# Optimization experiments

Hardware: AMD Instinct MI355X
Metric: run time of the kernel (lower is better)

## Reference

```python
import jax, jax.numpy as jnp
import numpy as np
import math

L, B, S, D, H, R = 4, 2, 1024, 1024, 16, 4
DH = D // H
SCALE = 1.0 / math.sqrt(DH)
EPS = 1e-5  # torch LayerNorm default


def _xavier(key, shape):
    fan_in, fan_out = shape[-2], shape[-1]
    bound = math.sqrt(6.0 / (fan_in + fan_out))
    return jax.random.uniform(key, shape, minval=-bound, maxval=bound, dtype=jnp.float32)


def setup_inputs() -> dict:
    key = jax.random.key(0)
    ks = jax.random.split(key, 12)
    f32 = jnp.float32
    return {
        "x": jax.random.normal(ks[0], (B, S, D), f32),
        "sigma": jnp.full((L,), 0.1, f32),
        "U": jax.random.normal(ks[1], (L, D, R), f32),
        "V": jax.random.normal(ks[2], (L, R, D), f32),
        "Wqkv1": _xavier(ks[3], (L, D, 3 * D)),
        "Wqkv2": _xavier(ks[4], (L, D, 3 * D)),
        "Wp1": _xavier(ks[5], (L, D // 2, D)),
        "bp1": jnp.zeros((L, D), f32),
        "Wp2": _xavier(ks[6], (L, D // 2, D)),
        "bp2": jnp.zeros((L, D), f32),
        "Wo": _xavier(ks[7], (L, D, D)),
        "bo": jnp.zeros((L, D), f32),
        "g_out": jnp.ones((L, D), f32), "b_out": jnp.zeros((L, D), f32),
        "g1": jnp.ones((L, D), f32), "b1": jnp.zeros((L, D), f32),
        "g2": jnp.ones((L, D), f32), "b2": jnp.zeros((L, D), f32),
        "Wm1": _xavier(ks[8], (L, D, 4 * D)),
        "bm1": jnp.zeros((L, 4 * D), f32),
        "Wm2": _xavier(ks[9], (L, 4 * D, D)),
        "bm2": jnp.zeros((L, D), f32),
        "gf": jnp.ones((D,), f32), "bf": jnp.zeros((D,), f32),
    }


def _ln(h, g, b):
    m = h.mean(-1, keepdims=True)
    v = ((h - m) ** 2).mean(-1, keepdims=True)
    return (h - m) * jax.lax.rsqrt(v + EPS) * g + b


def _heads(t):  # [B,S,D] -> [B,H,S,DH]
    return t.reshape(B, S, H, DH).transpose(0, 2, 1, 3)


def _forward(x, sigma, U, V, Wqkv1, Wqkv2, Wp1, bp1, Wp2, bp2, Wo, bo,
             g_out, b_out, g1, b1, g2, b2, Wm1, bm1, Wm2, bm2, gf, bf):
    params = (sigma, U, V, Wqkv1, Wqkv2, Wp1, bp1, Wp2, bp2, Wo, bo,
              g_out, b_out, g1, b1, g2, b2, Wm1, bm1, Wm2, bm2)

    def layer(xc, p):
        (sig, U_, V_, Wq1, Wq2, Wp1_, bp1_, Wp2_, bp2_, Wo_, bo_,
         gO, bO, g1_, b1_, g2_, b2_, Wm1_, bm1_, Wm2_, bm2_) = p
        h = _ln(xc, g1_, b1_)
        # svd_adapt = (sigma * (U @ V)).sum(-1) broadcast over batch/seq
        adapt = (sig * (U_ @ V_)).sum(-1)  # [D]
        a = h + adapt
        x1, x2 = jnp.split(a, 2, axis=-1)
        x1 = x1 @ Wp1_ + bp1_
        x2 = x2 @ Wp2_ + bp2_
        q1, k1, v1 = jnp.split(x1 @ Wq1, 3, axis=-1)
        q2, k2, v2 = jnp.split(x2 @ Wq2, 3, axis=-1)
        q1, k1, v1, q2, k2, v2 = map(_heads, (q1, k1, v1, q2, k2, v2))
        a1 = jax.nn.softmax(jnp.einsum('bhqd,bhkd->bhqk', q1, k1) * SCALE, axis=-1)
        a2 = jax.nn.softmax(jnp.einsum('bhqd,bhkd->bhqk', q2, k2) * SCALE, axis=-1)
        diff = a1 - a2
        # (diff@v1 + diff@v2)/2 == diff @ ((v1+v2)/2)
        out = jnp.einsum('bhqk,bhkd->bhqd', diff, (v1 + v2) * 0.5)
        out = out.transpose(0, 2, 1, 3).reshape(B, S, D)
        out = _ln(out @ Wo_ + bo_, gO, bO)
        xc = xc + out
        h2 = _ln(xc, g2_, b2_)
        xc = xc + (jax.nn.gelu(h2 @ Wm1_ + bm1_, approximate=False) @ Wm2_ + bm2_)
        return xc, None

    x, _ = jax.lax.scan(layer, x, params)
    return _ln(x, gf, bf)


def reference(x, sigma, U, V, Wqkv1, Wqkv2, Wp1, bp1, Wp2, bp2, Wo, bo,
              g_out, b_out, g1, b1, g2, b2, Wm1, bm1, Wm2, bm2, gf, bf):
    return _forward(x, sigma, U, V, Wqkv1, Wqkv2, Wp1, bp1, Wp2, bp2, Wo, bo,
                    g_out, b_out, g1, b1, g2, b2, Wm1, bm1, Wm2, bm2, gf, bf)
```

## Files before the change

### kernel.cpp

```cpp
#include <hip/hip_runtime.h>
#include <math.h>

typedef unsigned short u16;
typedef short bf16x8 __attribute__((ext_vector_type(8)));
typedef float f32x4 __attribute__((ext_vector_type(4)));

__device__ __forceinline__ float bf2f(u16 u){ return __uint_as_float(((unsigned)u)<<16); }
__device__ __forceinline__ u16 f2bf(float f){
  unsigned u = __float_as_uint(f);
  u += 0x7fffu + ((u>>16)&1u);
  return (u16)(u>>16);
}
__device__ __forceinline__ float gelu_f(float x){ return 0.5f*x*(1.0f+erff(x*0.7071067811865476f)); }

__device__ __forceinline__ void gload16(const void* g, void* l){
  __builtin_amdgcn_global_load_lds((const __attribute__((address_space(1))) void*)g,
                                   (__attribute__((address_space(3))) void*)l, 16, 0, 0);
}

__device__ __forceinline__ float block_sum(float v, float* sh){
  #pragma unroll
  for (int o=32;o;o>>=1) v += __shfl_down(v,o,64);
  int w = threadIdx.x>>6, lane = threadIdx.x&63;
  __syncthreads();
  if (lane==0) sh[w]=v;
  __syncthreads();
  return sh[0]+sh[1]+sh[2]+sh[3];
}

template<int FM,int FN,int OF32,int ACC,int ACT>
__global__ __launch_bounds__(256) void gemm2_k(
    const u16* __restrict__ A, const u16* __restrict__ Bm, void* __restrict__ Cv,
    const float* __restrict__ bias,
    int K,int lda,int ldb,int ldc,float alpha,int z0,
    long sAz,long oAb,long oAh, long sBz,long oBb,long oBh, long sCz,long oCb,long oCh)
{
  constexpr int BM = FM*32, BN = FN*32;
  int zz = blockIdx.z; int z = z0+zz; int bb = z>>4, hh = z&15;
  const u16* Ap = A  + (long)zz*sAz + (long)bb*oAb + (long)hh*oAh;
  const u16* Bp = Bm + (long)zz*sBz + (long)bb*oBb + (long)hh*oBh;
  long coff = (long)zz*sCz + (long)bb*oCb + (long)hh*oCh;
  int m0 = blockIdx.y*BM, n0 = blockIdx.x*BN;
  __shared__ __align__(16) u16 As[BM][64];
  __shared__ __align__(16) u16 Bs[BN][64];
  u16* AsF = &As[0][0]; u16* BsF = &Bs[0][0];
  int tid = threadIdx.x, w = tid>>6, l = tid&63;
  int q = l>>4, m16 = l&15;
  int wr = w>>1, wc = w&1;
  int sr  = w*8 + (l>>3);
  int sch = (l&7) ^ ((l>>3)&7);
  int s7  = m16 & 7;

  f32x4 acc[FM][FN];
  #pragma unroll
  for (int i=0;i<FM;i++)
    #pragma unroll
    for (int j=0;j<FN;j++) acc[i][j] = (f32x4){0.f,0.f,0.f,0.f};

  int aRow = wr*(FM*16) + m16;
  int bRow = wc*(FN*16) + m16;

  for (int k0=0;k0<K;k0+=64){
    __syncthreads();
    #pragma unroll
    for (int c=0;c<FM;c++)
      gload16(Ap + (long)(m0 + c*32 + sr)*lda + k0 + sch*8, AsF + c*2048 + w*512);
    #pragma unroll
    for (int c=0;c<FN;c++)
      gload16(Bp + (long)(n0 + c*32 + sr)*ldb + k0 + sch*8, BsF + c*2048 + w*512);
    __syncthreads();
    #pragma unroll
    for (int kh=0;kh<2;kh++){
      bf16x8 afr[FM], bfr[FN];
      #pragma unroll
      for (int i=0;i<FM;i++)
        afr[i] = *(const bf16x8*)(AsF + (aRow + i*16)*64 + (((kh<<2)|q) ^ s7)*8);
      #pragma unroll
      for (int j=0;j<FN;j++)
        bfr[j] = *(const bf16x8*)(BsF + (bRow + j*16)*64 + (((kh<<2)|q) ^ s7)*8);
      #pragma unroll
      for (int i=0;i<FM;i++)
        #pragma unroll
        for (int j=0;j<FN;j++)
          acc[i][j] = __builtin_amdgcn_mfma_f32_16x16x32_bf16(afr[i], bfr[j], acc[i][j], 0,0,0);
    }
  }
  #pragma unroll
  for (int j=0;j<FN;j++){
    int n = n0 + wc*(FN*16) + j*16 + m16;
    float bv = bias ? bias[n] : 0.0f;
    #pragma unroll
    for (int i=0;i<FM;i++){
      #pragma unroll
      for (int r=0;r<4;r++){
        int m = m0 + wr*(FM*16) + i*16 + q*4 + r;
        float v = acc[i][j][r]*alpha + bv;
        if (ACT==1) v = gelu_f(v);
        long ci = coff + (long)m*ldc + n;
        if (OF32){
          float* C = (float*)Cv;
          if (ACC) C[ci] += v; else C[ci] = v;
        } else {
          ((u16*)Cv)[ci] = f2bf(v);
        }
      }
    }
  }
}

__device__ __forceinline__ void flash_stream(
    const u16* Kl, const u16* Vl, u16* Plw,
    bf16x8 qa, bf16x8 qb, int qd, int m16,
    float& mrun, float& lsum, f32x4* O)
{
  int r7 = m16 & 7;
  f32x4 s[4];
  #pragma unroll
  for (int f=0;f<4;f++){
    s[f] = (f32x4){0.f,0.f,0.f,0.f};
    int row = f*16 + m16;
    bf16x8 ka = *(const bf16x8*)(Kl + row*64 + ((qd    ) ^ r7)*8);
    bf16x8 kb = *(const bf16x8*)(Kl + row*64 + ((4 + qd) ^ r7)*8);
    s[f] = __builtin_amdgcn_mfma_f32_16x16x32_bf16(ka, qa, s[f], 0,0,0);
    s[f] = __builtin_amdgcn_mfma_f32_16x16x32_bf16(kb, qb, s[f], 0,0,0);
  }
  float sc[16]; float pmax = -1e30f;
  #pragma unroll
  for (int f=0;f<4;f++)
    #pragma unroll
    for (int r=0;r<4;r++){ float v = s[f][r]*0.125f; sc[f*4+r]=v; pmax = fmaxf(pmax,v); }
  pmax = fmaxf(pmax, __shfl_xor(pmax,16,64));
  pmax = fmaxf(pmax, __shfl_xor(pmax,32,64));
  float mnew = fmaxf(mrun, pmax);
  float corr = expf(mrun - mnew);
  float psum = 0.f;
  #pragma unroll
  for (int f=0;f<4;f++){
    u16 pb[4];
    #pragma unroll
    for (int r=0;r<4;r++){ float e = expf(sc[f*4+r]-mnew); psum += e; pb[r] = f2bf(e); }
    unsigned lo = (unsigned)pb[0] | ((unsigned)pb[1]<<16);
    unsigned hi = (unsigned)pb[2] | ((unsigned)pb[3]<<16);
    uint2 pv; pv.x = lo; pv.y = hi;
    *(uint2*)(Plw + m16*72 + f*16 + qd*4) = pv;
  }
  psum += __shfl_xor(psum,16,64);
  psum += __shfl_xor(psum,32,64);
  lsum = lsum*corr + psum;
  mrun = mnew;
  float cO[4];
  #pragma unroll
  for (int r=0;r<4;r++) cO[r] = __shfl(corr, qd*4 + r, 64);
  #pragma unroll
  for (int f2=0;f2<4;f2++)
    #pragma unroll
    for (int r=0;r<4;r++) O[f2][r] *= cO[r];
  #pragma unroll
  for (int b32=0;b32<2;b32++){
    bf16x8 pa = *(const bf16x8*)(Plw + m16*72 + b32*32 + qd*8);
    #pragma unroll
    for (int f2=0;f2<4;f2++){
      int row = f2*16 + m16;
      bf16x8 vb = *(const bf16x8*)(Vl + row*64 + (((b32<<2)|qd) ^ r7)*8);
      O[f2] = __builtin_amdgcn_mfma_f32_16x16x32_bf16(pa, vb, O[f2], 0,0,0);
    }
  }
}

__global__ __launch_bounds__(256) void flash_k(
    const u16* __restrict__ qkv1, const u16* __restrict__ qkv2,
    const u16* __restrict__ vavgT, u16* __restrict__ outp)
{
  __shared__ __align__(16) u16 K1l[4096];
  __shared__ __align__(16) u16 K2l[4096];
  __shared__ __align__(16) u16 Vl[4096];
  __shared__ __align__(16) u16 Pl[4608];
  int z = blockIdx.y, b = z>>4, h = z&15;
  int q0 = blockIdx.x*64;
  int tid = threadIdx.x, w = tid>>6, l = tid&63;
  int qd = l>>4, m16 = l&15;
  int lr = l>>3;
  int sch = (l&7) ^ lr;
  u16* Plw = Pl + w*1152;

  const u16* q1p = qkv1 + ((long)(b*1024 + q0 + w*16 + m16))*3072 + h*64;
  const u16* q2p = qkv2 + ((long)(b*1024 + q0 + w*16 + m16))*3072 + h*64;
  bf16x8 q1a = *(const bf16x8*)(q1p + qd*8);
  bf16x8 q1b = *(const bf16x8*)(q1p + 32 + qd*8);
  bf16x8 q2a = *(const bf16x8*)(q2p + qd*8);
  bf16x8 q2b = *(const bf16x8*)(q2p + 32 + qd*8);

  const u16* k1base = qkv1 + ((long)(b*1024))*3072 + 1024 + h*64;
  const u16* k2base = qkv2 + ((long)(b*1024))*3072 + 1024 + h*64;
  const u16* vbase  = vavgT + (long)z*65536;

  float m1 = -1e30f, l1 = 0.f, m2 = -1e30f, l2 = 0.f;
  f32x4 O1[4], O2[4];
  #pragma unroll
  for (int f=0;f<4;f++){ O1[f]=(f32x4){0.f,0.f,0.f,0.f}; O2[f]=(f32x4){0.f,0.f,0.f,0.f}; }

  for (int t=0;t<16;t++){
    __syncthreads();
    #pragma unroll
    for (int c2=0;c2<2;c2++){
      int r = c2*32 + w*8 + lr;
      gload16(k1base + (long)(t*64 + r)*3072 + sch*8, K1l + c2*2048 + w*512);
      gload16(k2base + (long)(t*64 + r)*3072 + sch*8, K2l + c2*2048 + w*512);
      gload16(vbase  + (long)r*1024 + t*64 + sch*8,   Vl  + c2*2048 + w*512);
    }
    __syncthreads();
    flash_stream(K1l, Vl, Plw, q1a, q1b, qd, m16, m1, l1, O1);
    flash_stream(K2l, Vl, Plw, q2a, q2b, qd, m16, m2, l2, O2);
  }
  float inv1 = 1.0f/l1, inv2 = 1.0f/l2;
  float i1O[4], i2O[4];
  #pragma unroll
  for (int r=0;r<4;r++){ i1O[r] = __shfl(inv1, qd*4+r, 64); i2O[r] = __shfl(inv2, qd*4+r, 64); }
  #pragma unroll
  for (int f2=0;f2<4;f2++){
    #pragma unroll
    for (int r=0;r<4;r++){
      long idx = ((long)(b*1024 + q0 + w*16 + qd*4 + r))*1024 + h*64 + f2*16 + m16;
      outp[idx] = f2bf(O1[f2][r]*i1O[r] - O2[f2][r]*i2O[r]);
    }
  }
}

__global__ __launch_bounds__(256) void wtc_k(const float* __restrict__ in,
                                             u16* __restrict__ out, int N, int K){
  __shared__ float tile[64][65];
  int bx = blockIdx.x, by = blockIdx.y;
  int t = threadIdx.x, r = t>>6, c = t&63;
  const float* ip = in + (long)(by*64)*N + bx*64;
  #pragma unroll
  for (int i=0;i<16;i++) tile[i*4+r][c] = ip[(long)(i*4+r)*N + c];
  __syncthreads();
  u16* op = out + (long)(bx*64)*K + by*64;
  #pragma unroll
  for (int i=0;i<16;i++) op[(long)(i*4+r)*K + c] = f2bf(tile[c][i*4+r]);
}

template<int ACCXC,int HAS_OUT,int OUTF32>
__global__ __launch_bounds__(256) void ln_k(const float* __restrict__ in,
    const float* __restrict__ g, const float* __restrict__ b,
    float* __restrict__ xc, void* __restrict__ out)
{
  __shared__ float sh[4];
  long row = blockIdx.x;
  int tid = threadIdx.x;
  float x[4];
  #pragma unroll
  for (int i=0;i<4;i++) x[i] = in[row*1024 + tid + 256*i];
  float s = x[0]+x[1]+x[2]+x[3];
  float mean = block_sum(s, sh) * (1.0f/1024.0f);
  float ss = 0.f;
  #pragma unroll
  for (int i=0;i<4;i++){ float d = x[i]-mean; ss += d*d; }
  float var = block_sum(ss, sh) * (1.0f/1024.0f);
  float rstd = rsqrtf(var + 1e-5f);
  #pragma unroll
  for (int i=0;i<4;i++){
    int col = tid + 256*i;
    long idx = row*1024 + col;
    float val = (x[i]-mean)*rstd*g[col];
    if (b) val += b[col];
    if (ACCXC) xc[idx] += val;
    if (HAS_OUT){
      if (OUTF32) ((float*)out)[idx] = val;
      else ((u16*)out)[idx] = f2bf(val);
    }
  }
}

__global__ void cvt_k(const float* __restrict__ x, float* __restrict__ xc){
  long i = (long)blockIdx.x*256 + threadIdx.x;
  xc[i] = x[i];
}

__device__ __forceinline__ unsigned avg2(unsigned a, unsigned b){
  u16 r0 = f2bf(0.5f*(bf2f((u16)(a&0xffff)) + bf2f((u16)(b&0xffff))));
  u16 r1 = f2bf(0.5f*(bf2f((u16)(a>>16))    + bf2f((u16)(b>>16))));
  return (unsigned)r0 | ((unsigned)r1<<16);
}

__global__ __launch_bounds__(256) void vavg_k(const u16* __restrict__ qkv1,
                                              const u16* __restrict__ qkv2,
                                              u16* __restrict__ vavgT){
  __shared__ u16 tile[64][72];
  int z = blockIdx.y, b = z>>4, h = z&15;
  int s0 = blockIdx.x*64;
  int t = threadIdx.x, r = t>>2, seg = t&3;
  const u16* p1 = qkv1 + ((long)(b*1024 + s0 + r))*3072 + 2048 + h*64 + seg*16;
  const u16* p2 = qkv2 + ((long)(b*1024 + s0 + r))*3072 + 2048 + h*64 + seg*16;
  #pragma unroll
  for (int c=0;c<2;c++){
    uint4 a = *(const uint4*)(p1 + c*8);
    uint4 bb = *(const uint4*)(p2 + c*8);
    uint4 o; o.x = avg2(a.x,bb.x); o.y = avg2(a.y,bb.y); o.z = avg2(a.z,bb.z); o.w = avg2(a.w,bb.w);
    *(uint4*)&tile[r][seg*16 + c*8] = o;
  }
  __syncthreads();
  u16 ov[16];
  #pragma unroll
  for (int j=0;j<16;j++) ov[j] = tile[seg*16+j][r];
  uint4 w0, w1;
  w0.x = ov[0]|(ov[1]<<16);  w0.y = ov[2]|(ov[3]<<16);
  w0.z = ov[4]|(ov[5]<<16);  w0.w = ov[6]|(ov[7]<<16);
  w1.x = ov[8]|(ov[9]<<16);  w1.y = ov[10]|(ov[11]<<16);
  w1.z = ov[12]|(ov[13]<<16); w1.w = ov[14]|(ov[15]<<16);
  u16* op = vavgT + (long)z*65536 + (long)r*1024 + s0 + seg*16;
  *(uint4*)op = w0;
  *(uint4*)(op+8) = w1;
}

__global__ void abar_k(const float* __restrict__ sig, const float* __restrict__ U,
                       const float* __restrict__ V, const float* __restrict__ b1,
                       float* __restrict__ abar){
  __shared__ float vs[4];
  int tid = threadIdx.x, w = tid>>6, lane = tid&63;
  float p = 0.f;
  #pragma unroll
  for (int i=0;i<16;i++) p += V[w*1024 + lane + 64*i];
  #pragma unroll
  for (int o=32;o;o>>=1) p += __shfl_down(p,o,64);
  if (lane==0) vs[w] = p;
  __syncthreads();
  float sg = sig[0];
  for (int d=tid; d<1024; d+=256){
    float a = 0.f;
    #pragma unroll
    for (int r=0;r<4;r++) a += U[d*4+r]*vs[r];
    abar[d] = b1[d] + sg*a;
  }
}

__global__ void bar1p_k(const float* __restrict__ abar,
                        const float* __restrict__ Wp1, const float* __restrict__ Wp2,
                        float* __restrict__ bp){
  int n = blockIdx.x*256 + threadIdx.x;
  int kc = blockIdx.y;
  float s1=0.f, s2=0.f;
  for (int j=0;j<32;j++){
    int k = kc*32+j;
    s1 += abar[k]     * Wp1[(long)k*1024 + n];
    s2 += abar[512+k] * Wp2[(long)k*1024 + n];
  }
  bp[kc*2048 + n] = s1; bp[kc*2048 + 1024 + n] = s2;
}
__global__ void bar1r_k(const float* __restrict__ bp,
                        const float* __restrict__ bp1, const float* __restrict__ bp2,
                        float* __restrict__ x1bar, float* __restrict__ x2bar){
  int n = blockIdx.x*256 + threadIdx.x;
  float s1 = bp1[n], s2 = bp2[n];
  for (int kc=0;kc<16;kc++){ s1 += bp[kc*2048+n]; s2 += bp[kc*2048+1024+n]; }
  x1bar[n] = s1; x2bar[n] = s2;
}
__global__ void bar2p_k(const float* __restrict__ xbar, const float* __restrict__ Wq,
                        float* __restrict__ qp){
  int n = blockIdx.x*256 + threadIdx.x;
  int kc = blockIdx.y;
  float s = 0.f;
  for (int j=0;j<32;j++){
    int k = kc*32+j;
    s += xbar[k] * Wq[(long)k*3072 + n];
  }
  qp[kc*1024 + n] = s;
}
__global__ void bar2r_k(const float* __restrict__ qp, float* __restrict__ qbias){
  int m = blockIdx.x*256 + threadIdx.x;
  float s = 0.f;
  if (m < 1024){ for (int kc=0;kc<32;kc++) s += qp[kc*1024 + m]; }
  qbias[m] = s;
}

extern "C" void kernel_launch(void* const* d_in, const int* in_sizes, int n_in,
                              void* d_out, int out_size, void* d_ws, size_t ws_size,
                              hipStream_t stream){
  const float* X    = (const float*)d_in[0];
  const float* SIG  = (const float*)d_in[1];
  const float* U    = (const float*)d_in[2];
  const float* V    = (const float*)d_in[3];
  const float* Wqkv1= (const float*)d_in[4];
  const float* Wqkv2= (const float*)d_in[5];
  const float* Wp1  = (const float*)d_in[6];
  const float* bp1  = (const float*)d_in[7];
  const float* Wp2  = (const float*)d_in[8];
  const float* bp2  = (const float*)d_in[9];
  const float* Wo   = (const float*)d_in[10];
  const float* bo   = (const float*)d_in[11];
  const float* gO   = (const float*)d_in[12];
  const float* bO   = (const float*)d_in[13];
  const float* g1   = (const float*)d_in[14];
  const float* b1   = (const float*)d_in[15];
  const float* g2   = (const float*)d_in[16];
  const float* b2   = (const float*)d_in[17];
  const float* Wm1  = (const float*)d_in[18];
  const float* bm1  = (const float*)d_in[19];
  const float* Wm2  = (const float*)d_in[20];
  const float* bm2  = (const float*)d_in[21];
  const float* gf   = (const float*)d_in[22];
  const float* bfv  = (const float*)d_in[23];
  (void)in_sizes; (void)n_in; (void)out_size; (void)ws_size;

  char* p = (char*)d_ws;
  float* xc     = (float*)(p + 0);
  u16* qkv1     = (u16*)(p + 8388608);
  u16* qkv2     = (u16*)(p + 20971520);
  u16* bufA     = (u16*)(p + 33554432);
  u16* bufB     = (u16*)(p + 37748736);
  u16* bufC     = (u16*)(p + 41943040);
  u16* mid      = (u16*)(p + 46137344);
  float* projout= (float*)(p + 46137344);
  float* abar   = (float*)(p + 71303168);
  float* x1bar  = (float*)(p + 71307264);
  float* x2bar  = (float*)(p + 71311360);
  u16* wpT1     = (u16*)(p + 46137344);
  u16* wpT2     = (u16*)(p + 46137344 + 1048576);
  u16* wqkvT1   = (u16*)(p + 46137344 + 2097152);
  u16* wqkvT2   = (u16*)(p + 46137344 + 8388608);
  float* qbias1 = (float*)(p + 46137344 + 14680064);
  float* qbias2 = (float*)(p + 46137344 + 14692352);
  u16* woT      = (u16*)(p + 8388608);
  u16* wm1T     = (u16*)(p + 8388608 + 2097152);
  u16* wm2T     = (u16*)(p + 8388608 + 10485760);
  float* bp     = (float*)(p + 62914560);
  float* qp     = (float*)(p + 62914560 + 131072);

  u16* a_bf    = bufA; u16* attnout = bufA; u16* h2 = bufA;
  u16* x1w     = bufB;
  u16* x2w     = bufC; u16* vavgT   = bufC;

  cvt_k<<<8192,256,0,stream>>>(X, xc);
  for (int l=0;l<4;l++){
    abar_k<<<1,256,0,stream>>>(SIG+l, U+(long)l*4096, V+(long)l*4096, b1+l*1024, abar);
    bar1p_k<<<dim3(4,16),256,0,stream>>>(abar, Wp1+(long)l*524288, Wp2+(long)l*524288, bp);
    bar1r_k<<<4,256,0,stream>>>(bp, bp1+l*1024, bp2+l*1024, x1bar, x2bar);
    bar2p_k<<<dim3(4,32),256,0,stream>>>(x1bar, Wqkv1+(long)l*3145728, qp);
    bar2r_k<<<12,256,0,stream>>>(qp, qbias1);
    bar2p_k<<<dim3(4,32),256,0,stream>>>(x2bar, Wqkv2+(long)l*3145728, qp);
    bar2r_k<<<12,256,0,stream>>>(qp, qbias2);
    wtc_k<<<dim3(16,8), 256,0,stream>>>(Wp1+(long)l*524288,  wpT1, 1024, 512);
    wtc_k<<<dim3(16,8), 256,0,stream>>>(Wp2+(long)l*524288,  wpT2, 1024, 512);
    wtc_k<<<dim3(48,16),256,0,stream>>>(Wqkv1+(long)l*3145728, wqkvT1, 3072, 1024);
    wtc_k<<<dim3(48,16),256,0,stream>>>(Wqkv2+(long)l*3145728, wqkvT2, 3072, 1024);
    ln_k<0,1,0><<<2048,256,0,stream>>>(xc, g1+l*1024, nullptr, nullptr, a_bf);
    gemm2_k<2,4,0,0,0><<<dim3(8,32,1),256,0,stream>>>(a_bf,     wpT1, x1w, nullptr,
        512, 1024, 512, 1024, 1.0f, 0, 0,0,0, 0,0,0, 0,0,0);
    gemm2_k<2,4,0,0,0><<<dim3(8,32,1),256,0,stream>>>(a_bf+512, wpT2, x2w, nullptr,
        512, 1024, 512, 1024, 1.0f, 0, 0,0,0, 0,0,0, 0,0,0);
    gemm2_k<4,4,0,0,0><<<dim3(24,16,1),256,0,stream>>>(x1w, wqkvT1, qkv1, qbias1,
        1024, 1024, 1024, 3072, 1.0f, 0, 0,0,0, 0,0,0, 0,0,0);
    gemm2_k<4,4,0,0,0><<<dim3(24,16,1),256,0,stream>>>(x2w, wqkvT2, qkv2, qbias2,
        1024, 1024, 1024, 3072, 1.0f, 0, 0,0,0, 0,0,0, 0,0,0);
    vavg_k<<<dim3(16,32),256,0,stream>>>(qkv1,qkv2,vavgT);
    flash_k<<<dim3(16,32),256,0,stream>>>(qkv1, qkv2, vavgT, attnout);
    wtc_k<<<dim3(16,16),256,0,stream>>>(Wo +(long)l*1048576, woT,  1024, 1024);
    wtc_k<<<dim3(64,16),256,0,stream>>>(Wm1+(long)l*4194304, wm1T, 4096, 1024);
    wtc_k<<<dim3(16,64),256,0,stream>>>(Wm2+(long)l*4194304, wm2T, 1024, 4096);
    gemm2_k<2,4,1,0,0><<<dim3(8,32,1),256,0,stream>>>(attnout, woT, projout, bo+l*1024,
        1024, 1024, 1024, 1024, 1.0f, 0, 0,0,0, 0,0,0, 0,0,0);
    ln_k<1,0,0><<<2048,256,0,stream>>>(projout, gO+l*1024, bO+l*1024, xc, nullptr);
    ln_k<0,1,0><<<2048,256,0,stream>>>(xc, g2+l*1024, b2+l*1024, nullptr, h2);
    gemm2_k<4,4,0,0,1><<<dim3(32,16,1),256,0,stream>>>(h2, wm1T, mid, bm1+l*4096,
        1024, 1024, 1024, 4096, 1.0f, 0, 0,0,0, 0,0,0, 0,0,0);
    gemm2_k<2,4,1,1,0><<<dim3(8,32,1),256,0,stream>>>(mid, wm2T, (void*)xc, bm2+l*1024,
        4096, 4096, 4096, 1024, 1.0f, 0, 0,0,0, 0,0,0, 0,0,0);
  }
  ln_k<0,1,1><<<2048,256,0,stream>>>(xc, gf, bfv, nullptr, (float*)d_out);
}
```

Before: 1.586 ms.

## Batch paired projections, fold V-averaging into GEMM, and streamline flash softmax

The paired Wp and QKV GEMMs and the weight transposes now run as single launches over blockIdx.z. The separate vavg kernel is removed. The averaged V is produced transposed by a GEMM of the combined V weights against the concatenated x1/x2 activations with alpha 0.5, and the QK projection GEMMs no longer compute the V columns. The flash softmax switches to exp2 with a prescaled constant, uses packed bf16 conversion, and skips rescaling unless the running max grows by more than a threshold. It also raises wave priority around the MFMA sections. These changes cut launch count, skip redundant work, and reduce per-tile softmax ALU cost, at the risk of numerical drift from the lazy rescale.

```diff
diff --git a/kernel.cpp b/kernel.cpp
--- a/kernel.cpp
+++ b/kernel.cpp
@@ -12,6 +12,10 @@
   return (u16)(u>>16);
 }
 __device__ __forceinline__ float gelu_f(float x){ return 0.5f*x*(1.0f+erff(x*0.7071067811865476f)); }
+
+__device__ __forceinline__ unsigned cvtpk_bf16(float a, float b){
+  unsigned r; asm("v_cvt_pk_bf16_f32 %0, %1, %2" : "=v"(r) : "v"(a), "v"(b)); return r;
+}
 
 __device__ __forceinline__ void gload16(const void* g, void* l){
   __builtin_amdgcn_global_load_lds((const __attribute__((address_space(1))) void*)g,
@@ -31,15 +35,15 @@
 template<int FM,int FN,int OF32,int ACC,int ACT>
 __global__ __launch_bounds__(256) void gemm2_k(
     const u16* __restrict__ A, const u16* __restrict__ Bm, void* __restrict__ Cv,
-    const float* __restrict__ bias,
-    int K,int lda,int ldb,int ldc,float alpha,int z0,
-    long sAz,long oAb,long oAh, long sBz,long oBb,long oBh, long sCz,long oCb,long oCh)
+    const float* __restrict__ bias, int biasz,
+    int K,int lda,int ldb,int ldc,float alpha,
+    long sAz,long sBz,long sCz)
 {
   constexpr int BM = FM*32, BN = FN*32;
-  int zz = blockIdx.z; int z = z0+zz; int bb = z>>4, hh = z&15;
-  const u16* Ap = A  + (long)zz*sAz + (long)bb*oAb + (long)hh*oAh;
-  const u16* Bp = Bm + (long)zz*sBz + (long)bb*oBb + (long)hh*oBh;
-  long coff = (long)zz*sCz + (long)bb*oCb + (long)hh*oCh;
+  int zz = blockIdx.z;
+  const u16* Ap = A  + (long)zz*sAz;
+  const u16* Bp = Bm + (long)zz*sBz;
+  long coff = (long)zz*sCz;
   int m0 = blockIdx.y*BM, n0 = blockIdx.x*BN;
   __shared__ __align__(16) u16 As[BM][64];
   __shared__ __align__(16) u16 Bs[BN][64];
@@ -88,7 +92,7 @@
   #pragma unroll
   for (int j=0;j<FN;j++){
     int n = n0 + wc*(FN*16) + j*16 + m16;
-    float bv = bias ? bias[n] : 0.0f;
+    float bv = bias ? bias[(long)zz*biasz + n] : 0.0f;
     #pragma unroll
     for (int i=0;i<FM;i++){
       #pragma unroll
@@ -115,6 +119,7 @@
 {
   int r7 = m16 & 7;
   f32x4 s[4];
+  __builtin_amdgcn_s_setprio(1);
   #pragma unroll
   for (int f=0;f<4;f++){
     s[f] = (f32x4){0.f,0.f,0.f,0.f};
@@ -124,37 +129,43 @@
     s[f] = __builtin_amdgcn_mfma_f32_16x16x32_bf16(ka, qa, s[f], 0,0,0);
     s[f] = __builtin_amdgcn_mfma_f32_16x16x32_bf16(kb, qb, s[f], 0,0,0);
   }
+  __builtin_amdgcn_s_setprio(0);
+  const float SC2 = 0.18033688011112042f;
   float sc[16]; float pmax = -1e30f;
   #pragma unroll
   for (int f=0;f<4;f++)
     #pragma unroll
-    for (int r=0;r<4;r++){ float v = s[f][r]*0.125f; sc[f*4+r]=v; pmax = fmaxf(pmax,v); }
+    for (int r=0;r<4;r++){ float v = s[f][r]*SC2; sc[f*4+r]=v; pmax = fmaxf(pmax,v); }
   pmax = fmaxf(pmax, __shfl_xor(pmax,16,64));
   pmax = fmaxf(pmax, __shfl_xor(pmax,32,64));
-  float mnew = fmaxf(mrun, pmax);
-  float corr = expf(mrun - mnew);
+  bool resc = __any(pmax - mrun > 12.0f);
+  float mnew = resc ? fmaxf(mrun, pmax) : mrun;
   float psum = 0.f;
   #pragma unroll
   for (int f=0;f<4;f++){
-    u16 pb[4];
-    #pragma unroll
-    for (int r=0;r<4;r++){ float e = expf(sc[f*4+r]-mnew); psum += e; pb[r] = f2bf(e); }
-    unsigned lo = (unsigned)pb[0] | ((unsigned)pb[1]<<16);
-    unsigned hi = (unsigned)pb[2] | ((unsigned)pb[3]<<16);
-    uint2 pv; pv.x = lo; pv.y = hi;
+    float e0 = exp2f(sc[f*4+0]-mnew), e1 = exp2f(sc[f*4+1]-mnew);
+    float e2 = exp2f(sc[f*4+2]-mnew), e3 = exp2f(sc[f*4+3]-mnew);
+    psum += (e0+e1)+(e2+e3);
+    uint2 pv; pv.x = cvtpk_bf16(e0,e1); pv.y = cvtpk_bf16(e2,e3);
     *(uint2*)(Plw + m16*72 + f*16 + qd*4) = pv;
   }
   psum += __shfl_xor(psum,16,64);
   psum += __shfl_xor(psum,32,64);
-  lsum = lsum*corr + psum;
-  mrun = mnew;
-  float cO[4];
-  #pragma unroll
-  for (int r=0;r<4;r++) cO[r] = __shfl(corr, qd*4 + r, 64);
-  #pragma unroll
-  for (int f2=0;f2<4;f2++)
-    #pragma unroll
-    for (int r=0;r<4;r++) O[f2][r] *= cO[r];
+  if (resc){
+    float corr = exp2f(mrun - mnew);
+    lsum = lsum*corr + psum;
+    mrun = mnew;
+    float cO[4];
+    #pragma unroll
+    for (int r=0;r<4;r++) cO[r] = __shfl(corr, qd*4 + r, 64);
+    #pragma unroll
+    for (int f2=0;f2<4;f2++)
+      #pragma unroll
+      for (int r=0;r<4;r++) O[f2][r] *= cO[r];
+  } else {
+    lsum += psum;
+  }
+  __builtin_amdgcn_s_setprio(1);
   #pragma unroll
   for (int b32=0;b32<2;b32++){
     bf16x8 pa = *(const bf16x8*)(Plw + m16*72 + b32*32 + qd*8);
@@ -165,11 +176,12 @@
       O[f2] = __builtin_amdgcn_mfma_f32_16x16x32_bf16(pa, vb, O[f2], 0,0,0);
     }
   }
+  __builtin_amdgcn_s_setprio(0);
 }
 
 __global__ __launch_bounds__(256) void flash_k(
     const u16* __restrict__ qkv1, const u16* __restrict__ qkv2,
-    const u16* __restrict__ vavgT, u16* __restrict__ outp)
+    const u16* __restrict__ vavgC, u16* __restrict__ outp)
 {
   __shared__ __align__(16) u16 K1l[4096];
   __shared__ __align__(16) u16 K2l[4096];
@@ -183,16 +195,16 @@
   int sch = (l&7) ^ lr;
   u16* Plw = Pl + w*1152;
 
-  const u16* q1p = qkv1 + ((long)(b*1024 + q0 + w*16 + m16))*3072 + h*64;
-  const u16* q2p = qkv2 + ((long)(b*1024 + q0 + w*16 + m16))*3072 + h*64;
+  const u16* q1p = qkv1 + ((long)(b*1024 + q0 + w*16 + m16))*2048 + h*64;
+  const u16* q2p = qkv2 + ((long)(b*1024 + q0 + w*16 + m16))*2048 + h*64;
   bf16x8 q1a = *(const bf16x8*)(q1p + qd*8);
   bf16x8 q1b = *(const bf16x8*)(q1p + 32 + qd*8);
   bf16x8 q2a = *(const bf16x8*)(q2p + qd*8);
   bf16x8 q2b = *(const bf16x8*)(q2p + 32 + qd*8);
 
-  const u16* k1base = qkv1 + ((long)(b*1024))*3072 + 1024 + h*64;
-  const u16* k2base = qkv2 + ((long)(b*1024))*3072 + 1024 + h*64;
-  const u16* vbase  = vavgT + (long)z*65536;
+  const u16* k1base = qkv1 + ((long)(b*1024))*2048 + 1024 + h*64;
+  const u16* k2base = qkv2 + ((long)(b*1024))*2048 + 1024 + h*64;
+  const u16* vbase  = vavgC + (long)(h*64)*2048 + b*1024;
 
   float m1 = -1e30f, l1 = 0.f, m2 = -1e30f, l2 = 0.f;
   f32x4 O1[4], O2[4];
@@ -204,9 +216,9 @@
     #pragma unroll
     for (int c2=0;c2<2;c2++){
       int r = c2*32 + w*8 + lr;
-      gload16(k1base + (long)(t*64 + r)*3072 + sch*8, K1l + c2*2048 + w*512);
-      gload16(k2base + (long)(t*64 + r)*3072 + sch*8, K2l + c2*2048 + w*512);
-      gload16(vbase  + (long)r*1024 + t*64 + sch*8,   Vl  + c2*2048 + w*512);
+      gload16(k1base + (long)(t*64 + r)*2048 + sch*8, K1l + c2*2048 + w*512);
+      gload16(k2base + (long)(t*64 + r)*2048 + sch*8, K2l + c2*2048 + w*512);
+      gload16(vbase  + (long)r*2048 + t*64 + sch*8,   Vl  + c2*2048 + w*512);
     }
     __syncthreads();
     flash_stream(K1l, Vl, Plw, q1a, q1b, qd, m16, m1, l1, O1);
@@ -226,18 +238,23 @@
   }
 }
 
-__global__ __launch_bounds__(256) void wtc_k(const float* __restrict__ in,
-                                             u16* __restrict__ out, int N, int K){
+__global__ __launch_bounds__(256) void wtc_k(
+    const float* __restrict__ in0, const float* __restrict__ in1,
+    u16* __restrict__ out0, u16* __restrict__ out1,
+    int stride, int ldout, int koff0, int koff1){
+  const float* in = blockIdx.z ? in1 : in0;
+  u16* out = blockIdx.z ? out1 : out0;
+  int koff = blockIdx.z ? koff1 : koff0;
   __shared__ float tile[64][65];
   int bx = blockIdx.x, by = blockIdx.y;
   int t = threadIdx.x, r = t>>6, c = t&63;
-  const float* ip = in + (long)(by*64)*N + bx*64;
-  #pragma unroll
-  for (int i=0;i<16;i++) tile[i*4+r][c] = ip[(long)(i*4+r)*N + c];
+  const float* ip = in + (long)(by*64)*stride + bx*64;
+  #pragma unroll
+  for (int i=0;i<16;i++) tile[i*4+r][c] = ip[(long)(i*4+r)*stride + c];
   __syncthreads();
-  u16* op = out + (long)(bx*64)*K + by*64;
-  #pragma unroll
-  for (int i=0;i<16;i++) op[(long)(i*4+r)*K + c] = f2bf(tile[c][i*4+r]);
+  u16* op = out + (long)(bx*64)*ldout + by*64 + koff;
+  #pragma unroll
+  for (int i=0;i<16;i++) op[(long)(i*4+r)*ldout + c] = f2bf(tile[c][i*4+r]);
 }
 
 template<int ACCXC,int HAS_OUT,int OUTF32>
@@ -275,42 +292,6 @@
 __global__ void cvt_k(const float* __restrict__ x, float* __restrict__ xc){
   long i = (long)blockIdx.x*256 + threadIdx.x;
   xc[i] = x[i];
-}
-
-__device__ __forceinline__ unsigned avg2(unsigned a, unsigned b){
-  u16 r0 = f2bf(0.5f*(bf2f((u16)(a&0xffff)) + bf2f((u16)(b&0xffff))));
-  u16 r1 = f2bf(0.5f*(bf2f((u16)(a>>16))    + bf2f((u16)(b>>16))));
-  return (unsigned)r0 | ((unsigned)r1<<16);
-}
-
-__global__ __launch_bounds__(256) void vavg_k(const u16* __restrict__ qkv1,
-                                              const u16* __restrict__ qkv2,
-                                              u16* __restrict__ vavgT){
-  __shared__ u16 tile[64][72];
-  int z = blockIdx.y, b = z>>4, h = z&15;
-  int s0 = blockIdx.x*64;
-  int t = threadIdx.x, r = t>>2, seg = t&3;
-  const u16* p1 = qkv1 + ((long)(b*1024 + s0 + r))*3072 + 2048 + h*64 + seg*16;
-  const u16* p2 = qkv2 + ((long)(b*1024 + s0 + r))*3072 + 2048 + h*64 + seg*16;
-  #pragma unroll
-  for (int c=0;c<2;c++){
-    uint4 a = *(const uint4*)(p1 + c*8);
-    uint4 bb = *(const uint4*)(p2 + c*8);
-    uint4 o; o.x = avg2(a.x,bb.x); o.y = avg2(a.y,bb.y); o.z = avg2(a.z,bb.z); o.w = avg2(a.w,bb.w);
-    *(uint4*)&tile[r][seg*16 + c*8] = o;
-  }
-  __syncthreads();
-  u16 ov[16];
-  #pragma unroll
-  for (int j=0;j<16;j++) ov[j] = tile[seg*16+j][r];
-  uint4 w0, w1;
-  w0.x = ov[0]|(ov[1]<<16);  w0.y = ov[2]|(ov[3]<<16);
-  w0.z = ov[4]|(ov[5]<<16);  w0.w = ov[6]|(ov[7]<<16);
-  w1.x = ov[8]|(ov[9]<<16);  w1.y = ov[10]|(ov[11]<<16);
-  w1.z = ov[12]|(ov[13]<<16); w1.w = ov[14]|(ov[15]<<16);
-  u16* op = vavgT + (long)z*65536 + (long)r*1024 + s0 + seg*16;
-  *(uint4*)op = w0;
-  *(uint4*)(op+8) = w1;
 }
 
 __global__ void abar_k(const float* __restrict__ sig, const float* __restrict__ U,
@@ -355,21 +336,24 @@
   for (int kc=0;kc<16;kc++){ s1 += bp[kc*2048+n]; s2 += bp[kc*2048+1024+n]; }
   x1bar[n] = s1; x2bar[n] = s2;
 }
-__global__ void bar2p_k(const float* __restrict__ xbar, const float* __restrict__ Wq,
+__global__ void bar2p_k(const float* __restrict__ x1bar, const float* __restrict__ x2bar,
+                        const float* __restrict__ Wq1, const float* __restrict__ Wq2,
                         float* __restrict__ qp){
   int n = blockIdx.x*256 + threadIdx.x;
   int kc = blockIdx.y;
-  float s = 0.f;
+  float s1 = 0.f, s2 = 0.f;
   for (int j=0;j<32;j++){
     int k = kc*32+j;
-    s += xbar[k] * Wq[(long)k*3072 + n];
-  }
-  qp[kc*1024 + n] = s;
+    s1 += x1bar[k] * Wq1[(long)k*3072 + n];
+    s2 += x2bar[k] * Wq2[(long)k*3072 + n];
+  }
+  qp[kc*1024 + n] = s1; qp[32768 + kc*1024 + n] = s2;
 }
 __global__ void bar2r_k(const float* __restrict__ qp, float* __restrict__ qbias){
   int m = blockIdx.x*256 + threadIdx.x;
+  int st = m>>11, n = m&2047;
   float s = 0.f;
-  if (m < 1024){ for (int kc=0;kc<32;kc++) s += qp[kc*1024 + m]; }
+  if (n < 1024){ for (int kc=0;kc<32;kc++) s += qp[st*32768 + kc*1024 + n]; }
   qbias[m] = s;
 }
 
@@ -402,69 +386,65 @@
   const float* bfv  = (const float*)d_in[23];
   (void)in_sizes; (void)n_in; (void)out_size; (void)ws_size;
 
+  const long MB = 1024*1024;
   char* p = (char*)d_ws;
-  float* xc     = (float*)(p + 0);
-  u16* qkv1     = (u16*)(p + 8388608);
-  u16* qkv2     = (u16*)(p + 20971520);
-  u16* bufA     = (u16*)(p + 33554432);
-  u16* bufB     = (u16*)(p + 37748736);
-  u16* bufC     = (u16*)(p + 41943040);
-  u16* mid      = (u16*)(p + 46137344);
-  float* projout= (float*)(p + 46137344);
-  float* abar   = (float*)(p + 71303168);
-  float* x1bar  = (float*)(p + 71307264);
-  float* x2bar  = (float*)(p + 71311360);
-  u16* wpT1     = (u16*)(p + 46137344);
-  u16* wpT2     = (u16*)(p + 46137344 + 1048576);
-  u16* wqkvT1   = (u16*)(p + 46137344 + 2097152);
-  u16* wqkvT2   = (u16*)(p + 46137344 + 8388608);
-  float* qbias1 = (float*)(p + 46137344 + 14680064);
-  float* qbias2 = (float*)(p + 46137344 + 14692352);
-  u16* woT      = (u16*)(p + 8388608);
-  u16* wm1T     = (u16*)(p + 8388608 + 2097152);
-  u16* wm2T     = (u16*)(p + 8388608 + 10485760);
-  float* bp     = (float*)(p + 62914560);
-  float* qp     = (float*)(p + 62914560 + 131072);
-
-  u16* a_bf    = bufA; u16* attnout = bufA; u16* h2 = bufA;
-  u16* x1w     = bufB;
-  u16* x2w     = bufC; u16* vavgT   = bufC;
+  float* xc    = (float*)(p);
+  u16* qkv1    = (u16*)(p + 8*MB);
+  u16* qkv2    = (u16*)(p + 16*MB);
+  u16* bufA    = (u16*)(p + 24*MB);
+  u16* x12w    = (u16*)(p + 28*MB);
+  u16* vavgC   = (u16*)(p + 36*MB);
+  float* bp    = (float*)(p + 36*MB);
+  float* qp    = (float*)(p + 36*MB + 131072);
+  u16* wpT1    = (u16*)(p + 40*MB);
+  u16* wqkvT1  = (u16*)(p + 42*MB);
+  u16* wqkvT2  = (u16*)(p + 46*MB);
+  u16* wvT12   = (u16*)(p + 50*MB);
+  u16* mid     = (u16*)(p + 40*MB);
+  float* projout=(float*)(p + 56*MB);
+  float* qbias = (float*)(p + 56*MB);
+  u16* woT     = (u16*)(p + 8*MB);
+  u16* wm1T    = (u16*)(p + 10*MB);
+  u16* wm2T    = (u16*)(p + 28*MB);
+  float* abar  = (float*)(p + 64*MB);
+  float* x1bar = (float*)(p + 64*MB + 4096);
+  float* x2bar = (float*)(p + 64*MB + 8192);
+
+  u16* a_bf = bufA; u16* attnout = bufA; u16* h2 = bufA;
+  u16* wpT2 = wpT1 + 524288;
 
   cvt_k<<<8192,256,0,stream>>>(X, xc);
   for (int l=0;l<4;l++){
+    const float* Wqkv1l = Wqkv1+(long)l*3145728;
+    const float* Wqkv2l = Wqkv2+(long)l*3145728;
     abar_k<<<1,256,0,stream>>>(SIG+l, U+(long)l*4096, V+(long)l*4096, b1+l*1024, abar);
     bar1p_k<<<dim3(4,16),256,0,stream>>>(abar, Wp1+(long)l*524288, Wp2+(long)l*524288, bp);
     bar1r_k<<<4,256,0,stream>>>(bp, bp1+l*1024, bp2+l*1024, x1bar, x2bar);
-    bar2p_k<<<dim3(4,32),256,0,stream>>>(x1bar, Wqkv1+(long)l*3145728, qp);
-    bar2r_k<<<12,256,0,stream>>>(qp, qbias1);
-    bar2p_k<<<dim3(4,32),256,0,stream>>>(x2bar, Wqkv2+(long)l*3145728, qp);
-    bar2r_k<<<12,256,0,stream>>>(qp, qbias2);
-    wtc_k<<<dim3(16,8), 256,0,stream>>>(Wp1+(long)l*524288,  wpT1, 1024, 512);
-    wtc_k<<<dim3(16,8), 256,0,stream>>>(Wp2+(long)l*524288,  wpT2, 1024, 512);
-    wtc_k<<<dim3(48,16),256,0,stream>>>(Wqkv1+(long)l*3145728, wqkvT1, 3072, 1024);
-    wtc_k<<<dim3(48,16),256,0,stream>>>(Wqkv2+(long)l*3145728, wqkvT2, 3072, 1024);
+    bar2p_k<<<dim3(4,32),256,0,stream>>>(x1bar, x2bar, Wqkv1l, Wqkv2l, qp);
+    bar2r_k<<<16,256,0,stream>>>(qp, qbias);
+    wtc_k<<<dim3(16,8,2), 256,0,stream>>>(Wp1+(long)l*524288, Wp2+(long)l*524288,
+                                          wpT1, wpT2, 1024, 512, 0, 0);
+    wtc_k<<<dim3(32,16,2),256,0,stream>>>(Wqkv1l, Wqkv2l, wqkvT1, wqkvT2, 3072, 1024, 0, 0);
+    wtc_k<<<dim3(16,16,2),256,0,stream>>>(Wqkv1l+2048, Wqkv2l+2048, wvT12, wvT12, 3072, 2048, 0, 1024);
     ln_k<0,1,0><<<2048,256,0,stream>>>(xc, g1+l*1024, nullptr, nullptr, a_bf);
-    gemm2_k<2,4,0,0,0><<<dim3(8,32,1),256,0,stream>>>(a_bf,     wpT1, x1w, nullptr,
-        512, 1024, 512, 1024, 1.0f, 0, 0,0,0, 0,0,0, 0,0,0);
-    gemm2_k<2,4,0,0,0><<<dim3(8,32,1),256,0,stream>>>(a_bf+512, wpT2, x2w, nullptr,
-        512, 1024, 512, 1024, 1.0f, 0, 0,0,0, 0,0,0, 0,0,0);
-    gemm2_k<4,4,0,0,0><<<dim3(24,16,1),256,0,stream>>>(x1w, wqkvT1, qkv1, qbias1,
-        1024, 1024, 1024, 3072, 1.0f, 0, 0,0,0, 0,0,0, 0,0,0);
-    gemm2_k<4,4,0,0,0><<<dim3(24,16,1),256,0,stream>>>(x2w, wqkvT2, qkv2, qbias2,
-        1024, 1024, 1024, 3072, 1.0f, 0, 0,0,0, 0,0,0, 0,0,0);
-    vavg_k<<<dim3(16,32),256,0,stream>>>(qkv1,qkv2,vavgT);
-    flash_k<<<dim3(16,32),256,0,stream>>>(qkv1, qkv2, vavgT, attnout);
-    wtc_k<<<dim3(16,16),256,0,stream>>>(Wo +(long)l*1048576, woT,  1024, 1024);
-    wtc_k<<<dim3(64,16),256,0,stream>>>(Wm1+(long)l*4194304, wm1T, 4096, 1024);
-    wtc_k<<<dim3(16,64),256,0,stream>>>(Wm2+(long)l*4194304, wm2T, 1024, 4096);
-    gemm2_k<2,4,1,0,0><<<dim3(8,32,1),256,0,stream>>>(attnout, woT, projout, bo+l*1024,
-        1024, 1024, 1024, 1024, 1.0f, 0, 0,0,0, 0,0,0, 0,0,0);
+    gemm2_k<4,4,0,0,0><<<dim3(8,16,2),256,0,stream>>>(a_bf, wpT1, x12w, nullptr, 0,
+        512, 1024, 512, 2048, 1.0f, 512, 524288, 1024);
+    gemm2_k<4,4,0,0,0><<<dim3(16,16,2),256,0,stream>>>(x12w, wqkvT1, qkv1, qbias, 2048,
+        1024, 2048, 1024, 2048, 1.0f, 1024, 2097152, 4194304);
+    gemm2_k<4,4,0,0,0><<<dim3(16,8,1),256,0,stream>>>(wvT12, x12w, vavgC, nullptr, 0,
+        2048, 2048, 2048, 2048, 0.5f, 0, 0, 0);
+    flash_k<<<dim3(16,32),256,0,stream>>>(qkv1, qkv2, vavgC, attnout);
+    wtc_k<<<dim3(16,16,1),256,0,stream>>>(Wo +(long)l*1048576, nullptr, woT,  nullptr, 1024, 1024, 0, 0);
+    wtc_k<<<dim3(64,16,1),256,0,stream>>>(Wm1+(long)l*4194304, nullptr, wm1T, nullptr, 4096, 1024, 0, 0);
+    wtc_k<<<dim3(16,64,1),256,0,stream>>>(Wm2+(long)l*4194304, nullptr, wm2T, nullptr, 1024, 4096, 0, 0);
+    gemm2_k<2,4,1,0,0><<<dim3(8,32,1),256,0,stream>>>(attnout, woT, projout, bo+l*1024, 0,
+        1024, 1024, 1024, 1024, 1.0f, 0, 0, 0);
     ln_k<1,0,0><<<2048,256,0,stream>>>(projout, gO+l*1024, bO+l*1024, xc, nullptr);
     ln_k<0,1,0><<<2048,256,0,stream>>>(xc, g2+l*1024, b2+l*1024, nullptr, h2);
-    gemm2_k<4,4,0,0,1><<<dim3(32,16,1),256,0,stream>>>(h2, wm1T, mid, bm1+l*4096,
-        1024, 1024, 1024, 4096, 1.0f, 0, 0,0,0, 0,0,0, 0,0,0);
-    gemm2_k<2,4,1,1,0><<<dim3(8,32,1),256,0,stream>>>(mid, wm2T, (void*)xc, bm2+l*1024,
-        4096, 4096, 4096, 1024, 1.0f, 0, 0,0,0, 0,0,0, 0,0,0);
+    gemm2_k<4,4,0,0,1><<<dim3(32,16,1),256,0,stream>>>(h2, wm1T, mid, bm1+l*4096, 0,
+        1024, 1024, 1024, 4096, 1.0f, 0, 0, 0);
+    gemm2_k<2,4,1,1,0><<<dim3(8,32,1),256,0,stream>>>(mid, wm2T, (void*)xc, bm2+l*1024, 0,
+        4096, 4096, 4096, 1024, 1.0f, 0, 0, 0);
   }
   ln_k<0,1,1><<<2048,256,0,stream>>>(xc, gf, bfv, nullptr, (float*)d_out);
 }
```

Measured after the change: 1.514 ms. -4.5%, faster.
